# Kernel optimization log

Measured on AMD Instinct MI355X. Metric: run time of the kernel, lower is better.

Reference implementation:

```python
import jax, jax.numpy as jnp
import numpy as np

B, P, M, N, H, K, EH = 16, 50, 512, 1024, 64, 20, 200


def setup_inputs() -> dict:
    key = jax.random.key(0)
    ks = jax.random.split(key, 16)
    b = jax.random.normal(ks[0], (B, P, M, 1), jnp.float32)
    A = jax.random.normal(ks[1], (1, P, M, N), jnp.float32) / np.float32(np.sqrt(M))
    # random undirected multigraph on P nodes, stored with both directions
    s = jax.random.randint(ks[2], (B, EH), 0, P)
    off = jax.random.randint(ks[3], (B, EH), 1, P)
    d = (s + off) % P
    edge_index = jnp.stack([jnp.concatenate([s, d], 1), jnp.concatenate([d, s], 1)], 1).astype(jnp.int32)  # [B,2,2*EH]

    def lin(k, fi, fo, scale=None):
        scale = np.float32(1.0 / np.sqrt(fi)) if scale is None else np.float32(scale)
        return jax.random.normal(k, (fi, fo), jnp.float32) * scale, jnp.zeros((fo,), jnp.float32)

    W_e1, b_e1 = lin(ks[4], P * M, P * H)
    W_e2, b_e2 = lin(ks[5], P * H, 2 * P * H)
    W_e3, b_e3 = lin(ks[6], 2 * P * H, 4 * P * H)
    W_c1, b_c1 = lin(ks[7], 4 * H, 2 * H)
    W_c2, b_c2 = lin(ks[8], 2 * H, 2 * H)
    W_f1, b_f1 = lin(ks[9], 2 * H, H)
    W_f2, _ = lin(ks[10], H, K * 4, scale=1e-3)
    b_f2 = jnp.full((K * 4,), -2.0, jnp.float32)  # mimics fc2 init (tiny weights, negative bias)
    max_param = jnp.array([0.01, 0.1, 0.1, 0.1], jnp.float32).reshape(1, 1, 1, 4)  # [alpha,tau,rho,eta]_max
    y0 = jax.random.normal(ks[11], (B, P, N, 1), jnp.float32) * 0.01
    u0 = jax.random.normal(ks[12], (B, P, N, 1), jnp.float32) * 0.01
    d0 = jax.random.normal(ks[13], (B, P, N, 1), jnp.float32) * 0.01
    return dict(b=b, A=A, edge_index=edge_index, max_param=max_param,
                W_e1=W_e1, b_e1=b_e1, W_e2=W_e2, b_e2=b_e2, W_e3=W_e3, b_e3=b_e3,
                W_c1=W_c1, b_c1=b_c1, W_c2=W_c2, b_c2=b_c2,
                W_f1=W_f1, b_f1=b_f1, W_f2=W_f2, b_f2=b_f2,
                y0=y0, u0=u0, d0=d0)


def _lrelu(x):
    return jax.nn.leaky_relu(x, 0.01)


def _gcn(x, s, d, W, bias):
    # GCNConv: sym-normalized propagation with self loops. x: [P,F]
    h = x @ W
    deg = jnp.zeros((x.shape[0],), x.dtype).at[d].add(1.0) + 1.0  # +1 self loop
    dinv = jax.lax.rsqrt(deg)
    agg = jnp.zeros_like(h).at[d].add(h[s] * (dinv[s] * dinv[d])[:, None])
    agg = agg + h * (dinv * dinv)[:, None]  # self-loop term
    return agg + bias


def _delta(y, s, d):
    # nested neighbor loop: for each directed edge (s,d): delta[s]+=y[s]-y[d]; delta[d]-=same
    diff = y[s] - y[d]  # [E,N,1]
    return jnp.zeros_like(y).at[s].add(diff).at[d].add(-diff)


def reference(b, A, edge_index, max_param,
              W_e1, b_e1, W_e2, b_e2, W_e3, b_e3,
              W_c1, b_c1, W_c2, b_c2, W_f1, b_f1, W_f2, b_f2,
              y0, u0, d0):
    Bb = b.shape[0]
    n = A.shape[3]
    k_steps = W_f2.shape[1] // 4
    src, dst = edge_index[:, 0], edge_index[:, 1]

    # ---- GNN hypernetwork ----
    x = b.reshape(Bb, -1)
    x = _lrelu(x @ W_e1 + b_e1)
    x = _lrelu(x @ W_e2 + b_e2)
    x = (x @ W_e3 + b_e3).reshape(Bb, P, -1)  # [B,P,4H]
    x = _lrelu(jax.vmap(lambda xf, s, d: _gcn(xf, s, d, W_c1, b_c1))(x, src, dst))
    x = _lrelu(jax.vmap(lambda xf, s, d: _gcn(xf, s, d, W_c2, b_c2))(x, src, dst))
    x = x.mean(axis=1)  # global_mean_pool over nodes
    x = _lrelu(x @ W_f1 + b_f1)
    hyp = (x @ W_f2 + b_f2).reshape(Bb, k_steps, 1, 4)
    hyp = jax.nn.sigmoid(jnp.cumsum(hyp, axis=1)) * max_param  # [B,K,1,4]
    hyp_scan = jnp.transpose(hyp, (1, 3, 0, 2))[..., None, None]  # [K,4,B,1,1,1]

    # ---- precompute ----
    A0 = A[0]  # [P,M,N]
    AtA = jnp.einsum('pmn,pmk->pnk', A0, A0)  # [P,N,N]
    Atb = jnp.einsum('pmn,bpmo->bpno', A0, b)  # [B,P,N,1]
    sum_nb = jax.vmap(lambda s: jnp.zeros((P,), b.dtype).at[s].add(1.0))(src)[:, :, None, None]  # [B,P,1,1]

    # ---- unrolled D-ADMM / DLASSO ----
    def step(carry, hk):
        y_k, U_k, dlt = carry
        alpha, tau, rho, eta = hk[0], hk[1], hk[2], hk[3]
        AtAy = jnp.einsum('pnk,bpko->bpno', AtA, y_k)
        g = AtAy - Atb + jnp.sign(y_k) * tau + U_k * sum_nb + dlt * rho
        y_n = y_k - alpha * g
        dlt_n = jax.vmap(_delta)(y_n, src, dst)
        U_n = U_k + dlt_n * eta
        return (y_n, U_n, dlt_n), y_n

    _, Y = jax.lax.scan(step, (y0, u0, d0), hyp_scan)
    return Y  # [K,B,P,N,1]
```

## Files before the change

### kernel.cpp

```cpp
#include <hip/hip_runtime.h>

namespace {
constexpr int NB = 16;
constexpr int NP = 50;
constexpr int NM = 512;
constexpr int NN = 1024;
constexpr int NK = 20;
constexpr long ASZ = (long)NP * NM * NN;
constexpr long YSZ = (long)NB * NP * NN;
}

typedef __attribute__((ext_vector_type(8))) short bf16x8;
typedef __attribute__((ext_vector_type(4))) float f32x4;

__device__ __forceinline__ float lrelu(float x){ return x > 0.f ? x : 0.01f*x; }
__device__ __forceinline__ unsigned short f2bf(float f){
  unsigned u = __builtin_bit_cast(unsigned, f);
  u += 0x7fffu + ((u >> 16) & 1u);
  return (unsigned short)(u >> 16);
}

__global__ __launch_bounds__(256) void k_prep(const float* __restrict__ A,
                      unsigned short* __restrict__ abfT){
  const int p = blockIdx.x, mt = blockIdx.y, nt = blockIdx.z;
  const int tid = threadIdx.x;
  __shared__ unsigned short tile[64][72];
  const int m0 = mt*64, n0 = nt*64;
  {
    int r = tid>>2, cs = (tid&3)*16;
    const float* src = A + ((long)p*NM + m0 + r)*NN + n0 + cs;
    unsigned short tmp[16];
    #pragma unroll
    for (int q=0;q<16;q+=4){
      float4 v = *(const float4*)(src+q);
      tmp[q+0]=f2bf(v.x); tmp[q+1]=f2bf(v.y); tmp[q+2]=f2bf(v.z); tmp[q+3]=f2bf(v.w);
    }
    #pragma unroll
    for (int q=0;q<16;q++) tile[r][cs+q] = tmp[q];
  }
  __syncthreads();
  {
    int r = tid>>2, cs = (tid&3)*16;
    unsigned short* dst = abfT + ((long)p*NN + n0 + r)*NM + m0 + cs;
    unsigned short tmp[16];
    #pragma unroll
    for (int q=0;q<16;q++) tmp[q] = tile[cs+q][r];
    #pragma unroll
    for (int q=0;q<16;q+=8) *(uint4*)(dst+q) = *(const uint4*)&tmp[q];
  }
}

__global__ void k_init(const float* __restrict__ y0, const float* __restrict__ u0,
                       float* __restrict__ y, float* __restrict__ u,
                       unsigned short* __restrict__ ybf, int n){
  int e = (blockIdx.x*blockDim.x + threadIdx.x)*4;
  if (e >= n) return;
  float4 a = *(const float4*)(y0+e);
  *(float4*)(y+e) = a;
  ushort4 o; o.x=f2bf(a.x); o.y=f2bf(a.y); o.z=f2bf(a.z); o.w=f2bf(a.w);
  *(ushort4*)(ybf+e) = o;
  *(float4*)(u+e)  = *(const float4*)(u0+e);
}

__global__ __launch_bounds__(256) void k_c0(const float* __restrict__ u0,
      const float* __restrict__ d0, const float* __restrict__ snbg,
      const float* __restrict__ hypg, float* __restrict__ c){
  long e = ((long)blockIdx.x*256 + threadIdx.x)*4;
  if (e >= YSZ) return;
  long bp = e >> 10;
  int b = (int)(bp/NP), p = (int)(bp%NP);
  float sp = snbg[b*NP+p], rho = hypg[b*80 + 2];
  float4 uv = *(const float4*)(u0+e);
  float4 dv = *(const float4*)(d0+e);
  float4 cv;
  cv.x = uv.x*sp + dv.x*rho; cv.y = uv.y*sp + dv.y*rho;
  cv.z = uv.z*sp + dv.z*rho; cv.w = uv.w*sp + dv.w*rho;
  *(float4*)(c+e) = cv;
}

__global__ __launch_bounds__(256) void k_atb(const unsigned short* __restrict__ abfT,
                      const float* __restrict__ src, float* __restrict__ z){
  const int p = blockIdx.x;
  const int tid = threadIdx.x, wave = tid>>6, lane = tid&63;
  __shared__ unsigned short tlds[16][520];
  {
    int b = tid>>4, c0 = (tid&15)*8;
    const float* tr = src + ((long)b*NP + p)*NM;
    #pragma unroll
    for (int it=0; it<4; it++){
      float4 lo = *(const float4*)(tr + it*128 + c0);
      float4 hi = *(const float4*)(tr + it*128 + c0 + 4);
      unsigned short w[8];
      w[0]=f2bf(lo.x); w[1]=f2bf(lo.y); w[2]=f2bf(lo.z); w[3]=f2bf(lo.w);
      w[4]=f2bf(hi.x); w[5]=f2bf(hi.y); w[6]=f2bf(hi.z); w[7]=f2bf(hi.w);
      *(uint4*)&tlds[b][it*128 + c0] = *(const uint4*)w;
    }
  }
  __syncthreads();
  const int lr = lane&15, kg = lane>>4;
  const int nt0 = blockIdx.y*4 + wave;
  const int n0 = nt0*16, n1 = (nt0+32)*16;
  const unsigned short* b0 = abfT + ((long)p*NN + n0 + lr)*NM + kg*8;
  const unsigned short* b1 = abfT + ((long)p*NN + n1 + lr)*NM + kg*8;
  const unsigned short* tp = &tlds[lr][kg*8];
  f32x4 acc0a={0.f,0.f,0.f,0.f}, acc0b={0.f,0.f,0.f,0.f};
  f32x4 acc1a={0.f,0.f,0.f,0.f}, acc1b={0.f,0.f,0.f,0.f};
  #pragma unroll 4
  for (int ks=0; ks<16; ks+=2){
    bf16x8 t0 = *(const bf16x8*)(tp + ks*32);
    bf16x8 t1 = *(const bf16x8*)(tp + ks*32 + 32);
    bf16x8 b00 = *(const bf16x8*)(b0 + (long)ks*32);
    bf16x8 b01 = *(const bf16x8*)(b0 + (long)ks*32 + 32);
    bf16x8 b10 = *(const bf16x8*)(b1 + (long)ks*32);
    bf16x8 b11 = *(const bf16x8*)(b1 + (long)ks*32 + 32);
    acc0a = __builtin_amdgcn_mfma_f32_16x16x32_bf16(t0, b00, acc0a, 0, 0, 0);
    acc1a = __builtin_amdgcn_mfma_f32_16x16x32_bf16(t0, b10, acc1a, 0, 0, 0);
    acc0b = __builtin_amdgcn_mfma_f32_16x16x32_bf16(t1, b01, acc0b, 0, 0, 0);
    acc1b = __builtin_amdgcn_mfma_f32_16x16x32_bf16(t1, b11, acc1b, 0, 0, 0);
  }
  f32x4 acc0 = acc0a + acc0b;
  f32x4 acc1 = acc1a + acc1b;
  #pragma unroll
  for (int r=0;r<4;r++){
    int bb = kg*4 + r;
    z[((long)bb*NP + p)*NN + n0 + lr] = acc0[r];
    z[((long)bb*NP + p)*NN + n1 + lr] = acc1[r];
  }
}

__global__ __launch_bounds__(256) void k_ata(const unsigned short* __restrict__ abfT,
                      unsigned short* __restrict__ ata){
  const int p = blockIdx.x;
  int yy = blockIdx.y, bi = 0;
  while (yy >= 8 - bi){ yy -= 8 - bi; bi++; }
  const int bj = bi + yy;
  const int i0 = bi*128, j0 = bj*128;
  const int tid = threadIdx.x, wave = tid>>6, lane = tid&63;
  const int lr = lane&15, kg = lane>>4;
  __shared__ unsigned short pa[128][72];
  __shared__ unsigned short pb[128][72];
  f32x4 acc[2][8];
  #pragma unroll
  for (int ti=0;ti<2;ti++)
    #pragma unroll
    for (int tj=0;tj<8;tj++) acc[ti][tj] = (f32x4){0.f,0.f,0.f,0.f};
  const unsigned short* Abase = abfT + (long)p*NN*NM;
  for (int mc=0; mc<NM; mc+=64){
    __syncthreads();
    {
      int r = tid>>1, c0 = (tid&1)*32;
      const unsigned short* sa = Abase + (long)(i0 + r)*NM + mc + c0;
      const unsigned short* sb = Abase + (long)(j0 + r)*NM + mc + c0;
      #pragma unroll
      for (int q=0;q<32;q+=8){
        *(uint4*)&pa[r][c0+q] = *(const uint4*)(sa+q);
        *(uint4*)&pb[r][c0+q] = *(const uint4*)(sb+q);
      }
    }
    __syncthreads();
    #pragma unroll
    for (int ks=0; ks<2; ks++){
      bf16x8 av0 = *(const bf16x8*)&pa[wave*32      + lr][ks*32 + kg*8];
      bf16x8 av1 = *(const bf16x8*)&pa[wave*32 + 16 + lr][ks*32 + kg*8];
      #pragma unroll
      for (int tj=0;tj<8;tj++){
        bf16x8 bv = *(const bf16x8*)&pb[tj*16 + lr][ks*32 + kg*8];
        acc[0][tj] = __builtin_amdgcn_mfma_f32_16x16x32_bf16(av0, bv, acc[0][tj], 0,0,0);
        acc[1][tj] = __builtin_amdgcn_mfma_f32_16x16x32_bf16(av1, bv, acc[1][tj], 0,0,0);
      }
    }
  }
  const long pbase = (long)p << 20;
  #pragma unroll
  for (int ti=0; ti<2; ti++){
    const int ib = i0 + wave*32 + ti*16;
    #pragma unroll
    for (int tj=0; tj<8; tj++){
      const int jb = j0 + tj*16;
      unsigned short w[4];
      #pragma unroll
      for (int r=0;r<4;r++) w[r] = f2bf(acc[ti][tj][r]);
      #pragma unroll
      for (int r=0;r<4;r++)
        ata[pbase + (long)(ib + kg*4 + r)*1024 + jb + lr] = w[r];
      if (bi != bj)
        *(ushort4*)(ata + pbase + (long)(jb + lr)*1024 + ib + kg*4) = *(const ushort4*)w;
    }
  }
}

__global__ __launch_bounds__(256) void k_enc2(const float* __restrict__ X, const float* __restrict__ W,
                           float* __restrict__ part, int fi, int fo, int ichunk, int actin){
  const int tid = threadIdx.x;
  const int o0 = (blockIdx.x*256 + tid)*4;
  const int c  = blockIdx.y;
  const bool ok = o0 < fo;
  __shared__ float xs[64][16];
  float4 acc[16];
  #pragma unroll
  for (int b=0;b<16;b++){ acc[b].x=0.f; acc[b].y=0.f; acc[b].z=0.f; acc[b].w=0.f; }
  const long ibase = (long)c*ichunk;
  const int xb = tid&15, xio = (tid>>4)*4;
  for (int s=0; s<ichunk; s+=64){
    float4 v = *(const float4*)(X + (long)xb*fi + ibase + s + xio);
    if (actin){ v.x=lrelu(v.x); v.y=lrelu(v.y); v.z=lrelu(v.z); v.w=lrelu(v.w); }
    __syncthreads();
    xs[xio+0][xb]=v.x; xs[xio+1][xb]=v.y; xs[xio+2][xb]=v.z; xs[xio+3][xb]=v.w;
    __syncthreads();
    const float* wp = W + (ibase+s)*fo + o0;
    #pragma unroll 4
    for (int i=0;i<64;i++){
      float4 w;
      if (ok) w = *(const float4*)(wp + (long)i*fo);
      else { w.x=0.f; w.y=0.f; w.z=0.f; w.w=0.f; }
      #pragma unroll
      for (int b2=0;b2<16;b2+=4){
        float4 x4 = *(const float4*)&xs[i][b2];
        acc[b2+0].x += w.x*x4.x; acc[b2+0].y += w.y*x4.x; acc[b2+0].z += w.z*x4.x; acc[b2+0].w += w.w*x4.x;
        acc[b2+1].x += w.x*x4.y; acc[b2+1].y += w.y*x4.y; acc[b2+1].z += w.z*x4.y; acc[b2+1].w += w.w*x4.y;
        acc[b2+2].x += w.x*x4.z; acc[b2+2].y += w.y*x4.z; acc[b2+2].z += w.z*x4.z; acc[b2+2].w += w.w*x4.z;
        acc[b2+3].x += w.x*x4.w; acc[b2+3].y += w.y*x4.w; acc[b2+3].z += w.z*x4.w; acc[b2+3].w += w.w*x4.w;
      }
    }
  }
  if (ok){
    float* pp = part + ((long)c*16)*fo + o0;
    #pragma unroll
    for (int b=0;b<16;b++) *(float4*)(pp + (long)b*fo) = acc[b];
  }
}

__global__ void k_enc_reduce(const float* __restrict__ part, const float* __restrict__ bias,
                             float* __restrict__ out, int fo, int nchunk){
  int i = blockIdx.x*256 + threadIdx.x;
  if (i >= 16*fo) return;
  int o = i % fo;
  float s = bias[o];
  for (int c=0;c<nchunk;c++) s += part[(long)c*16*fo + i];
  out[i] = s;
}

__global__ __launch_bounds__(64) void k_graph(const int* __restrict__ ei, float* __restrict__ adjg,
                        float* __restrict__ dmg, float* __restrict__ snbg){
  const int b = blockIdx.x, tid = threadIdx.x;
  __shared__ float adj[2500], dm[2500], deg[50], dinv[50], snb[50];
  for (int i=tid;i<2500;i+=64){ adj[i]=0.f; dm[i]=0.f; }
  if (tid<50){ deg[tid]=0.f; snb[tid]=0.f; }
  __syncthreads();
  const int* e = ei + b*800;
  for (int k=tid;k<400;k+=64){
    atomicAdd(&deg[e[400+k]], 1.f);
    atomicAdd(&snb[e[k]], 1.f);
  }
  __syncthreads();
  if (tid<50) dinv[tid] = 1.f / sqrtf(deg[tid] + 1.f);
  __syncthreads();
  for (int k=tid;k<400;k+=64){
    int s = e[k], d = e[400+k];
    atomicAdd(&adj[d*50+s], dinv[s]*dinv[d]);
    atomicAdd(&dm[s*50+s],  1.f); atomicAdd(&dm[s*50+d], -1.f);
    atomicAdd(&dm[d*50+d],  1.f); atomicAdd(&dm[d*50+s], -1.f);
  }
  __syncthreads();
  if (tid<50) adj[tid*50+tid] += dinv[tid]*dinv[tid];
  __syncthreads();
  for (int i=tid;i<2500;i+=64){ adjg[b*2500+i]=adj[i]; dmg[b*2500+i]=dm[i]; }
  if (tid<50) snbg[b*50+tid]=snb[tid];
}

__global__ __launch_bounds__(256) void k_gnn(const float* __restrict__ h3,
     const float* __restrict__ Wc1, const float* __restrict__ bc1,
     const float* __restrict__ Wc2, const float* __restrict__ bc2,
     const float* __restrict__ Wf1, const float* __restrict__ bf1,
     const float* __restrict__ Wf2, const float* __restrict__ bf2,
     const float* __restrict__ maxp, const float* __restrict__ adjg,
     float* __restrict__ hypg){
  const int b = blockIdx.x, tid = threadIdx.x;
  __shared__ float adj[2500];
  __shared__ float bufA[6400];
  __shared__ float bufB[6400];
  __shared__ float xm[128], hv1[64], raw[80];
  for (int i=tid;i<2500;i+=256) adj[i] = adjg[b*2500+i];

  const int j = tid & 127, nh = tid >> 7;
  float acc[25];
  #pragma unroll
  for (int q=0;q<25;q++) acc[q]=0.f;
  for (int ic=0; ic<4; ic++){
    __syncthreads();
    for (int e=tid; e<800; e+=256){
      int n = e>>4, seg = (e&15)*4;
      *(float4*)&bufB[n*64+seg] = *(const float4*)(h3 + (long)b*12800 + n*256 + ic*64 + seg);
    }
    __syncthreads();
    for (int i=0;i<64;i+=4){
      float w0 = Wc1[(long)(ic*64+i+0)*128 + j];
      float w1 = Wc1[(long)(ic*64+i+1)*128 + j];
      float w2 = Wc1[(long)(ic*64+i+2)*128 + j];
      float w3 = Wc1[(long)(ic*64+i+3)*128 + j];
      #pragma unroll
      for (int q=0;q<25;q++){
        float4 xv = *(const float4*)&bufB[(nh*25+q)*64 + i];
        acc[q] += xv.x*w0 + xv.y*w1 + xv.z*w2 + xv.w*w3;
      }
    }
  }
  __syncthreads();
  #pragma unroll
  for (int q=0;q<25;q++) bufA[(nh*25+q)*128 + j] = acc[q];
  __syncthreads();
  {
    float a2[25];
    float bv = bc1[j];
    #pragma unroll
    for (int q=0;q<25;q++) a2[q]=bv;
    for (int qq=0; qq<50; qq++){
      float hvv = bufA[qq*128 + j];
      #pragma unroll
      for (int q=0;q<25;q++) a2[q] += adj[(nh*25+q)*50 + qq]*hvv;
    }
    __syncthreads();
    #pragma unroll
    for (int q=0;q<25;q++) bufB[(nh*25+q)*128 + j] = lrelu(a2[q]);
  }
  __syncthreads();
  {
    float a2[25];
    #pragma unroll
    for (int q=0;q<25;q++) a2[q]=0.f;
    for (int i=0;i<128;i+=4){
      float w0 = Wc2[(long)(i+0)*128 + j];
      float w1 = Wc2[(long)(i+1)*128 + j];
      float w2 = Wc2[(long)(i+2)*128 + j];
      float w3 = Wc2[(long)(i+3)*128 + j];
      #pragma unroll
      for (int q=0;q<25;q++){
        float4 xv = *(const float4*)&bufB[(nh*25+q)*128 + i];
        a2[q] += xv.x*w0 + xv.y*w1 + xv.z*w2 + xv.w*w3;
      }
    }
    __syncthreads();
    #pragma unroll
    for (int q=0;q<25;q++) bufA[(nh*25+q)*128 + j] = a2[q];
  }
  __syncthreads();
  {
    float a2[25];
    float bv = bc2[j];
    #pragma unroll
    for (int q=0;q<25;q++) a2[q]=bv;
    for (int qq=0; qq<50; qq++){
      float hvv = bufA[qq*128 + j];
      #pragma unroll
      for (int q=0;q<25;q++) a2[q] += adj[(nh*25+q)*50 + qq]*hvv;
    }
    __syncthreads();
    #pragma unroll
    for (int q=0;q<25;q++) bufB[(nh*25+q)*128 + j] = lrelu(a2[q]);
  }
  __syncthreads();
  if (tid < 128){
    float s = 0.f;
    for (int n=0;n<50;n++) s += bufB[n*128 + tid];
    xm[tid] = s * (1.f/50.f);
  }
  __syncthreads();
  if (tid < 64){
    float s = bf1[tid];
    for (int i=0;i<128;i++) s += xm[i]*Wf1[i*64 + tid];
    hv1[tid] = lrelu(s);
  }
  __syncthreads();
  if (tid < 80){
    float s = bf2[tid];
    for (int i=0;i<64;i++) s += hv1[i]*Wf2[i*80 + tid];
    raw[tid] = s;
  }
  __syncthreads();
  if (tid < 4){
    float c = 0.f;
    for (int k=0;k<20;k++){
      c += raw[k*4 + tid];
      hypg[b*80 + k*4 + tid] = maxp[tid] / (1.f + expf(-c));
    }
  }
}

__global__ __launch_bounds__(256) void k_z(const unsigned short* __restrict__ ata,
      const unsigned short* __restrict__ ybin, const float* __restrict__ atb,
      const float* __restrict__ cbuf, const float* __restrict__ hypg, int k,
      float* __restrict__ y, unsigned short* __restrict__ ybout,
      float* __restrict__ yout){
  const int p = blockIdx.x;
  const int tid = threadIdx.x, wave = tid>>6, lane = tid&63;
  __shared__ unsigned short ylds[16][1032];
  {
    int b = tid>>4, c0 = (tid&15)*8;
    const unsigned short* yr = ybin + ((long)b*NP + p)*NN;
    #pragma unroll
    for (int it=0; it<8; it++)
      *(uint4*)&ylds[b][it*128 + c0] = *(const uint4*)(yr + it*128 + c0);
  }
  const int lr = lane&15, kg = lane>>4;
  const int n0 = (blockIdx.y*4 + wave)*16;
  const long pb2 = (long)p << 20;
  const unsigned short* bp = ata + pb2 + (long)(n0 + lr)*1024 + kg*8;
  const unsigned short* yp = &ylds[lr][kg*8];

  float yv4[4], atb4[4], c4[4];
  float4 hp4[4];
  #pragma unroll
  for (int r=0;r<4;r++){
    const int b = kg*4 + r;
    const long idx = ((long)b*NP + p)*NN + n0 + lr;
    yv4[r] = y[idx]; atb4[r] = atb[idx]; c4[r] = cbuf[idx];
    hp4[r] = *(const float4*)(hypg + b*80 + k*4);
  }
  __syncthreads();

  f32x4 a0={0.f,0.f,0.f,0.f}, a1={0.f,0.f,0.f,0.f}, a2={0.f,0.f,0.f,0.f}, a3={0.f,0.f,0.f,0.f};
  #pragma unroll 4
  for (int i=0;i<8;i++){
    bf16x8 b0 = *(const bf16x8*)(bp + (i*4+0)*32);
    bf16x8 b1 = *(const bf16x8*)(bp + (i*4+1)*32);
    bf16x8 b2 = *(const bf16x8*)(bp + (i*4+2)*32);
    bf16x8 b3 = *(const bf16x8*)(bp + (i*4+3)*32);
    bf16x8 y0 = *(const bf16x8*)(yp + (i*4+0)*32);
    bf16x8 y1 = *(const bf16x8*)(yp + (i*4+1)*32);
    bf16x8 y2 = *(const bf16x8*)(yp + (i*4+2)*32);
    bf16x8 y3 = *(const bf16x8*)(yp + (i*4+3)*32);
    a0 = __builtin_amdgcn_mfma_f32_16x16x32_bf16(y0, b0, a0, 0,0,0);
    a1 = __builtin_amdgcn_mfma_f32_16x16x32_bf16(y1, b1, a1, 0,0,0);
    a2 = __builtin_amdgcn_mfma_f32_16x16x32_bf16(y2, b2, a2, 0,0,0);
    a3 = __builtin_amdgcn_mfma_f32_16x16x32_bf16(y3, b3, a3, 0,0,0);
  }
  f32x4 z = (a0 + a1) + (a2 + a3);
  #pragma unroll
  for (int r=0;r<4;r++){
    const int b = kg*4 + r;
    const long idx = ((long)b*NP + p)*NN + n0 + lr;
    float yv = yv4[r];
    float g = z[r] - atb4[r] + ((yv>0.f)?1.f:((yv<0.f)?-1.f:0.f))*hp4[r].y + c4[r];
    float ynv = yv - hp4[r].x*g;
    y[idx] = ynv; ybout[idx] = f2bf(ynv); yout[(long)k*YSZ + idx] = ynv;
  }
}

__global__ __launch_bounds__(256) void k_dm(const float* __restrict__ dmg,
      const float* __restrict__ snbg, const float* __restrict__ hypg, int k,
      const float* __restrict__ y, float* __restrict__ u, float* __restrict__ c){
  const int b = blockIdx.x, n0 = blockIdx.y*128, tid = threadIdx.x;
  __shared__ float ys[50][128];
  __shared__ float dms[2500];
  for (int i=tid;i<2500;i+=256) dms[i] = dmg[b*2500+i];
  for (int e=tid; e<6400; e+=256){
    int p=e>>7, nn=e&127;
    ys[p][nn] = y[((long)b*NP+p)*NN + n0 + nn];
  }
  __syncthreads();
  const float eta = hypg[b*80 + k*4 + 3];
  const float rhon = hypg[b*80 + (k+1)*4 + 2];
  for (int e=tid; e<6400; e+=256){
    int p=e>>7, nn=e&127;
    float s=0.f;
    #pragma unroll 10
    for (int q=0;q<NP;q++) s += dms[p*50+q]*ys[q][nn];
    long idx = ((long)b*NP+p)*NN + n0 + nn;
    float un = u[idx] + s*eta;
    u[idx] = un;
    c[idx] = un*snbg[b*NP+p] + s*rhon;
  }
}

extern "C" void kernel_launch(void* const* d_in, const int* in_sizes, int n_in,
                              void* d_out, int out_size, void* d_ws, size_t ws_size,
                              hipStream_t stream){
  (void)in_sizes; (void)n_in; (void)out_size; (void)ws_size;
  const float* bin = (const float*)d_in[0];
  const float* A   = (const float*)d_in[1];
  const int*   ei  = (const int*)d_in[2];
  const float* mxp = (const float*)d_in[3];
  const float* We1 = (const float*)d_in[4];  const float* be1 = (const float*)d_in[5];
  const float* We2 = (const float*)d_in[6];  const float* be2 = (const float*)d_in[7];
  const float* We3 = (const float*)d_in[8];  const float* be3 = (const float*)d_in[9];
  const float* Wc1 = (const float*)d_in[10]; const float* bc1 = (const float*)d_in[11];
  const float* Wc2 = (const float*)d_in[12]; const float* bc2 = (const float*)d_in[13];
  const float* Wf1 = (const float*)d_in[14]; const float* bf1 = (const float*)d_in[15];
  const float* Wf2 = (const float*)d_in[16]; const float* bf2 = (const float*)d_in[17];
  const float* y0  = (const float*)d_in[18];
  const float* u0  = (const float*)d_in[19];
  const float* dd0 = (const float*)d_in[20];
  float* out = (float*)d_out;

  char* cur = (char*)d_ws;
  auto alloc = [&](size_t bytes)->void*{
    void* pp = (void*)cur; cur += (bytes + 255) & ~(size_t)255; return pp;
  };
  unsigned short* abfT = (unsigned short*)alloc(ASZ*2);
  unsigned short* ata  = (unsigned short*)alloc((size_t)NP*1024*1024*2);
  float* atb = (float*)alloc(YSZ*4);
  float* y   = (float*)alloc(YSZ*4);
  unsigned short* ybf0 = (unsigned short*)alloc(YSZ*2);
  unsigned short* ybf1 = (unsigned short*)alloc(YSZ*2);
  float* u   = (float*)alloc(YSZ*4);
  float* cb  = (float*)alloc(YSZ*4);
  float* h1  = (float*)alloc((size_t)16*3200*4);
  float* h2  = (float*)alloc((size_t)16*6400*4);
  float* h3  = (float*)alloc((size_t)16*12800*4);
  float* adj = (float*)alloc((size_t)16*2500*4);
  float* dm  = (float*)alloc((size_t)16*2500*4);
  float* snb = (float*)alloc((size_t)16*50*4);
  float* hyp = (float*)alloc((size_t)16*80*4);
  float* part= (float*)alloc((size_t)84000000);

  k_prep<<<dim3(50,8,16), dim3(256), 0, stream>>>(A, abfT);
  k_init<<<dim3(800), dim3(256), 0, stream>>>(y0, u0, y, u, ybf0, (int)YSZ);
  k_atb<<<dim3(50,8), dim3(256), 0, stream>>>(abfT, bin, atb);
  k_ata<<<dim3(50,36), dim3(256), 0, stream>>>(abfT, ata);

  k_enc2<<<dim3(4,200),  dim3(256), 0, stream>>>(bin, We1, part, 25600, 3200, 128, 0);
  k_enc_reduce<<<dim3(200), dim3(256), 0, stream>>>(part, be1, h1, 3200, 200);
  k_enc2<<<dim3(7,50),  dim3(256), 0, stream>>>(h1, We2, part, 3200, 6400, 64, 1);
  k_enc_reduce<<<dim3(400), dim3(256), 0, stream>>>(part, be2, h2, 6400, 50);
  k_enc2<<<dim3(13,100), dim3(256), 0, stream>>>(h2, We3, part, 6400, 12800, 64, 1);
  k_enc_reduce<<<dim3(800), dim3(256), 0, stream>>>(part, be3, h3, 12800, 100);

  k_graph<<<dim3(16), dim3(64), 0, stream>>>(ei, adj, dm, snb);
  k_gnn<<<dim3(16), dim3(256), 0, stream>>>(h3, Wc1, bc1, Wc2, bc2, Wf1, bf1, Wf2, bf2, mxp, adj, hyp);
  k_c0<<<dim3(800), dim3(256), 0, stream>>>(u0, dd0, snb, hyp, cb);

  for (int k=0;k<NK;k++){
    const unsigned short* ybin = (k & 1) ? ybf1 : ybf0;
    unsigned short* ybout      = (k & 1) ? ybf0 : ybf1;
    k_z<<<dim3(50,16), dim3(256), 0, stream>>>(ata, ybin, atb, cb, hyp, k, y, ybout, out);
    if (k < NK-1)
      k_dm<<<dim3(16,8), dim3(256), 0, stream>>>(dm, snb, hyp, k, y, u, cb);
  }
}
```

Before: 1.530 ms.

## Fuse unrolled ADMM iterations into one persistent kernel with grid barriers

Replaces the per-iteration k_z and k_dm launches, plus the init and c0 kernels, with one persistent 800-block kernel. Blocks synchronise through a global atomic counter barrier, and y, u and atb stay in registers across the 20 steps. The delta (graph Laplacian) term is recomputed inside each block from the bf16 copy of y, which removes the fp32 y, u and c round-trips through memory. In exchange it relies on all 800 blocks being co-resident, otherwise the barrier deadlocks. It also does redundant per-block reads of the other nodes' y, and computes delta from bf16 rather than fp32 y, which lowers precision.

```diff
diff --git a/kernel.cpp b/kernel.cpp
--- a/kernel.cpp
+++ b/kernel.cpp
@@ -14,6 +14,10 @@
 typedef __attribute__((ext_vector_type(4))) float f32x4;
 
 __device__ __forceinline__ float lrelu(float x){ return x > 0.f ? x : 0.01f*x; }
+__device__ __forceinline__ float bfu(unsigned short x){
+  unsigned v = ((unsigned)x) << 16;
+  return __builtin_bit_cast(float, v);
+}
 __device__ __forceinline__ unsigned short f2bf(float f){
   unsigned u = __builtin_bit_cast(unsigned, f);
   u += 0x7fffu + ((u >> 16) & 1u);
@@ -50,33 +54,7 @@
   }
 }
 
-__global__ void k_init(const float* __restrict__ y0, const float* __restrict__ u0,
-                       float* __restrict__ y, float* __restrict__ u,
-                       unsigned short* __restrict__ ybf, int n){
-  int e = (blockIdx.x*blockDim.x + threadIdx.x)*4;
-  if (e >= n) return;
-  float4 a = *(const float4*)(y0+e);
-  *(float4*)(y+e) = a;
-  ushort4 o; o.x=f2bf(a.x); o.y=f2bf(a.y); o.z=f2bf(a.z); o.w=f2bf(a.w);
-  *(ushort4*)(ybf+e) = o;
-  *(float4*)(u+e)  = *(const float4*)(u0+e);
-}
-
-__global__ __launch_bounds__(256) void k_c0(const float* __restrict__ u0,
-      const float* __restrict__ d0, const float* __restrict__ snbg,
-      const float* __restrict__ hypg, float* __restrict__ c){
-  long e = ((long)blockIdx.x*256 + threadIdx.x)*4;
-  if (e >= YSZ) return;
-  long bp = e >> 10;
-  int b = (int)(bp/NP), p = (int)(bp%NP);
-  float sp = snbg[b*NP+p], rho = hypg[b*80 + 2];
-  float4 uv = *(const float4*)(u0+e);
-  float4 dv = *(const float4*)(d0+e);
-  float4 cv;
-  cv.x = uv.x*sp + dv.x*rho; cv.y = uv.y*sp + dv.y*rho;
-  cv.z = uv.z*sp + dv.z*rho; cv.w = uv.w*sp + dv.w*rho;
-  *(float4*)(c+e) = cv;
-}
+__global__ void k_zero(unsigned long long* cnt){ *cnt = 0ull; }
 
 __global__ __launch_bounds__(256) void k_atb(const unsigned short* __restrict__ abfT,
                       const float* __restrict__ src, float* __restrict__ z){
@@ -386,89 +364,117 @@
   }
 }
 
-__global__ __launch_bounds__(256) void k_z(const unsigned short* __restrict__ ata,
-      const unsigned short* __restrict__ ybin, const float* __restrict__ atb,
-      const float* __restrict__ cbuf, const float* __restrict__ hypg, int k,
-      float* __restrict__ y, unsigned short* __restrict__ ybout,
-      float* __restrict__ yout){
-  const int p = blockIdx.x;
+__device__ __forceinline__ void gridbar(unsigned long long* cnt, unsigned long long target){
+  __syncthreads();
+  if (threadIdx.x == 0){
+    __threadfence();
+    __hip_atomic_fetch_add(cnt, 1ull, __ATOMIC_ACQ_REL, __HIP_MEMORY_SCOPE_AGENT);
+    while (__hip_atomic_load(cnt, __ATOMIC_ACQUIRE, __HIP_MEMORY_SCOPE_AGENT) < target)
+      __builtin_amdgcn_s_sleep(8);
+    __threadfence();
+  }
+  __syncthreads();
+}
+
+__global__ __launch_bounds__(256, 4) void k_scan(
+      const unsigned short* __restrict__ ata, const float* __restrict__ atb_g,
+      const float* __restrict__ y0, const float* __restrict__ u0,
+      const float* __restrict__ d0, const float* __restrict__ dmg,
+      const float* __restrict__ snbg, const float* __restrict__ hypg,
+      unsigned short* __restrict__ yb0, unsigned short* __restrict__ yb1,
+      float* __restrict__ yout, unsigned long long* cnt){
+  const int p  = blockIdx.x >> 4;
+  const int nt = blockIdx.x & 15;
   const int tid = threadIdx.x, wave = tid>>6, lane = tid&63;
+  const int lr = lane&15, kg = lane>>4;
+  const int n  = nt*64 + wave*16 + lr;
   __shared__ unsigned short ylds[16][1032];
-  {
-    int b = tid>>4, c0 = (tid&15)*8;
-    const unsigned short* yr = ybin + ((long)b*NP + p)*NN;
-    #pragma unroll
-    for (int it=0; it<8; it++)
-      *(uint4*)&ylds[b][it*128 + c0] = *(const uint4*)(yr + it*128 + c0);
-  }
-  const int lr = lane&15, kg = lane>>4;
-  const int n0 = (blockIdx.y*4 + wave)*16;
-  const long pb2 = (long)p << 20;
-  const unsigned short* bp = ata + pb2 + (long)(n0 + lr)*1024 + kg*8;
-  const unsigned short* yp = &ylds[lr][kg*8];
-
-  float yv4[4], atb4[4], c4[4];
-  float4 hp4[4];
+  __shared__ float dmp[16][52];
+  __shared__ float snp[16];
+  for (int e = tid; e < 800; e += 256){
+    int b = e/50, q = e%50;
+    dmp[b][q] = dmg[b*2500 + p*50 + q];
+  }
+  if (tid < 16) snp[tid] = snbg[tid*NP + p];
+
+  float yv[4], uv[4], at4[4], ds[4];
   #pragma unroll
   for (int r=0;r<4;r++){
-    const int b = kg*4 + r;
-    const long idx = ((long)b*NP + p)*NN + n0 + lr;
-    yv4[r] = y[idx]; atb4[r] = atb[idx]; c4[r] = cbuf[idx];
-    hp4[r] = *(const float4*)(hypg + b*80 + k*4);
-  }
-  __syncthreads();
-
-  f32x4 a0={0.f,0.f,0.f,0.f}, a1={0.f,0.f,0.f,0.f}, a2={0.f,0.f,0.f,0.f}, a3={0.f,0.f,0.f,0.f};
-  #pragma unroll 4
-  for (int i=0;i<8;i++){
-    bf16x8 b0 = *(const bf16x8*)(bp + (i*4+0)*32);
-    bf16x8 b1 = *(const bf16x8*)(bp + (i*4+1)*32);
-    bf16x8 b2 = *(const bf16x8*)(bp + (i*4+2)*32);
-    bf16x8 b3 = *(const bf16x8*)(bp + (i*4+3)*32);
-    bf16x8 y0 = *(const bf16x8*)(yp + (i*4+0)*32);
-    bf16x8 y1 = *(const bf16x8*)(yp + (i*4+1)*32);
-    bf16x8 y2 = *(const bf16x8*)(yp + (i*4+2)*32);
-    bf16x8 y3 = *(const bf16x8*)(yp + (i*4+3)*32);
-    a0 = __builtin_amdgcn_mfma_f32_16x16x32_bf16(y0, b0, a0, 0,0,0);
-    a1 = __builtin_amdgcn_mfma_f32_16x16x32_bf16(y1, b1, a1, 0,0,0);
-    a2 = __builtin_amdgcn_mfma_f32_16x16x32_bf16(y2, b2, a2, 0,0,0);
-    a3 = __builtin_amdgcn_mfma_f32_16x16x32_bf16(y3, b3, a3, 0,0,0);
-  }
-  f32x4 z = (a0 + a1) + (a2 + a3);
-  #pragma unroll
-  for (int r=0;r<4;r++){
-    const int b = kg*4 + r;
-    const long idx = ((long)b*NP + p)*NN + n0 + lr;
-    float yv = yv4[r];
-    float g = z[r] - atb4[r] + ((yv>0.f)?1.f:((yv<0.f)?-1.f:0.f))*hp4[r].y + c4[r];
-    float ynv = yv - hp4[r].x*g;
-    y[idx] = ynv; ybout[idx] = f2bf(ynv); yout[(long)k*YSZ + idx] = ynv;
-  }
-}
-
-__global__ __launch_bounds__(256) void k_dm(const float* __restrict__ dmg,
-      const float* __restrict__ snbg, const float* __restrict__ hypg, int k,
-      const float* __restrict__ y, float* __restrict__ u, float* __restrict__ c){
-  const int b = blockIdx.x, n0 = blockIdx.y*128, tid = threadIdx.x;
-  __shared__ float ys[50][128];
-  __shared__ float dms[2500];
-  for (int i=tid;i<2500;i+=256) dms[i] = dmg[b*2500+i];
-  for (int e=tid; e<6400; e+=256){
-    int p=e>>7, nn=e&127;
-    ys[p][nn] = y[((long)b*NP+p)*NN + n0 + nn];
-  }
-  __syncthreads();
-  const float eta = hypg[b*80 + k*4 + 3];
-  const float rhon = hypg[b*80 + (k+1)*4 + 2];
-  for (int e=tid; e<6400; e+=256){
-    int p=e>>7, nn=e&127;
-    float s=0.f;
-    #pragma unroll 10
-    for (int q=0;q<NP;q++) s += dms[p*50+q]*ys[q][nn];
-    long idx = ((long)b*NP+p)*NN + n0 + nn;
-    float un = u[idx] + s*eta;
-    u[idx] = un;
-    c[idx] = un*snbg[b*NP+p] + s*rhon;
+    const int b = kg*4+r;
+    const long idx = ((long)b*NP + p)*NN + n;
+    yv[r]  = y0[idx];
+    uv[r]  = u0[idx];
+    at4[r] = atb_g[idx];
+    yb0[idx] = f2bf(yv[r]);
+  }
+  __threadfence();
+  gridbar(cnt, 800ull);
+
+  for (int k=0;k<NK;k++){
+    const unsigned short* ybin = (k&1) ? yb1 : yb0;
+    unsigned short*       ybot = (k&1) ? yb0 : yb1;
+    if (k == 0){
+      #pragma unroll
+      for (int r=0;r<4;r++)
+        ds[r] = d0[((long)(kg*4+r)*NP + p)*NN + n];
+    } else {
+      #pragma unroll
+      for (int r=0;r<4;r++) ds[r] = 0.f;
+      for (int q=0;q<NP;q++){
+        #pragma unroll
+        for (int r=0;r<4;r++){
+          float yq = bfu(ybin[((long)(kg*4+r)*NP + q)*NN + n]);
+          ds[r] += dmp[kg*4+r][q]*yq;
+        }
+      }
+      #pragma unroll
+      for (int r=0;r<4;r++)
+        uv[r] += hypg[(kg*4+r)*80 + (k-1)*4 + 3]*ds[r];
+    }
+    __syncthreads();
+    {
+      int bb = tid>>4, c0 = (tid&15)*8;
+      const unsigned short* yr = ybin + ((long)bb*NP + p)*NN;
+      #pragma unroll
+      for (int it=0; it<8; it++)
+        *(uint4*)&ylds[bb][it*128 + c0] = *(const uint4*)(yr + it*128 + c0);
+    }
+    __syncthreads();
+    const unsigned short* bp = ata + ((long)p<<20) + (long)(nt*64 + wave*16 + lr)*1024 + kg*8;
+    const unsigned short* yp = &ylds[lr][kg*8];
+    f32x4 a0={0.f,0.f,0.f,0.f}, a1={0.f,0.f,0.f,0.f}, a2={0.f,0.f,0.f,0.f}, a3={0.f,0.f,0.f,0.f};
+    #pragma unroll 2
+    for (int i=0;i<8;i++){
+      bf16x8 b0 = *(const bf16x8*)(bp + (i*4+0)*32);
+      bf16x8 b1 = *(const bf16x8*)(bp + (i*4+1)*32);
+      bf16x8 b2 = *(const bf16x8*)(bp + (i*4+2)*32);
+      bf16x8 b3 = *(const bf16x8*)(bp + (i*4+3)*32);
+      bf16x8 q0 = *(const bf16x8*)(yp + (i*4+0)*32);
+      bf16x8 q1 = *(const bf16x8*)(yp + (i*4+1)*32);
+      bf16x8 q2 = *(const bf16x8*)(yp + (i*4+2)*32);
+      bf16x8 q3 = *(const bf16x8*)(yp + (i*4+3)*32);
+      a0 = __builtin_amdgcn_mfma_f32_16x16x32_bf16(q0, b0, a0, 0,0,0);
+      a1 = __builtin_amdgcn_mfma_f32_16x16x32_bf16(q1, b1, a1, 0,0,0);
+      a2 = __builtin_amdgcn_mfma_f32_16x16x32_bf16(q2, b2, a2, 0,0,0);
+      a3 = __builtin_amdgcn_mfma_f32_16x16x32_bf16(q3, b3, a3, 0,0,0);
+    }
+    f32x4 z = (a0 + a1) + (a2 + a3);
+    #pragma unroll
+    for (int r=0;r<4;r++){
+      const int b = kg*4+r;
+      const float4 hp = *(const float4*)(hypg + b*80 + k*4);
+      float g = z[r] - at4[r] + ((yv[r]>0.f)?1.f:((yv[r]<0.f)?-1.f:0.f))*hp.y
+              + uv[r]*snp[b] + ds[r]*hp.z;
+      yv[r] -= hp.x*g;
+      yout[(long)k*YSZ + ((long)b*NP+p)*NN + n] = yv[r];
+    }
+    if (k < NK-1){
+      #pragma unroll
+      for (int r=0;r<4;r++)
+        ybot[((long)(kg*4+r)*NP + p)*NN + n] = f2bf(yv[r]);
+      __threadfence();
+      gridbar(cnt, (unsigned long long)(k+2)*800ull);
+    }
   }
 }
 
@@ -499,11 +505,8 @@
   unsigned short* abfT = (unsigned short*)alloc(ASZ*2);
   unsigned short* ata  = (unsigned short*)alloc((size_t)NP*1024*1024*2);
   float* atb = (float*)alloc(YSZ*4);
-  float* y   = (float*)alloc(YSZ*4);
   unsigned short* ybf0 = (unsigned short*)alloc(YSZ*2);
   unsigned short* ybf1 = (unsigned short*)alloc(YSZ*2);
-  float* u   = (float*)alloc(YSZ*4);
-  float* cb  = (float*)alloc(YSZ*4);
   float* h1  = (float*)alloc((size_t)16*3200*4);
   float* h2  = (float*)alloc((size_t)16*6400*4);
   float* h3  = (float*)alloc((size_t)16*12800*4);
@@ -511,10 +514,11 @@
   float* dm  = (float*)alloc((size_t)16*2500*4);
   float* snb = (float*)alloc((size_t)16*50*4);
   float* hyp = (float*)alloc((size_t)16*80*4);
+  unsigned long long* cnt = (unsigned long long*)alloc(256);
   float* part= (float*)alloc((size_t)84000000);
 
+  k_zero<<<dim3(1), dim3(1), 0, stream>>>(cnt);
   k_prep<<<dim3(50,8,16), dim3(256), 0, stream>>>(A, abfT);
-  k_init<<<dim3(800), dim3(256), 0, stream>>>(y0, u0, y, u, ybf0, (int)YSZ);
   k_atb<<<dim3(50,8), dim3(256), 0, stream>>>(abfT, bin, atb);
   k_ata<<<dim3(50,36), dim3(256), 0, stream>>>(abfT, ata);
 
@@ -527,13 +531,7 @@
 
   k_graph<<<dim3(16), dim3(64), 0, stream>>>(ei, adj, dm, snb);
   k_gnn<<<dim3(16), dim3(256), 0, stream>>>(h3, Wc1, bc1, Wc2, bc2, Wf1, bf1, Wf2, bf2, mxp, adj, hyp);
-  k_c0<<<dim3(800), dim3(256), 0, stream>>>(u0, dd0, snb, hyp, cb);
-
-  for (int k=0;k<NK;k++){
-    const unsigned short* ybin = (k & 1) ? ybf1 : ybf0;
-    unsigned short* ybout      = (k & 1) ? ybf0 : ybf1;
-    k_z<<<dim3(50,16), dim3(256), 0, stream>>>(ata, ybin, atb, cb, hyp, k, y, ybout, out);
-    if (k < NK-1)
-      k_dm<<<dim3(16,8), dim3(256), 0, stream>>>(dm, snb, hyp, k, y, u, cb);
-  }
-}
+
+  k_scan<<<dim3(800), dim3(256), 0, stream>>>(ata, atb, y0, u0, dd0, dm, snb, hyp,
+                                              ybf0, ybf1, out, cnt);
+}
```

Measured after the change: 5.770 ms. +277.3%, slower.

## Prefetch AtA tiles in k_z, read bf16 y in k_dm, reorder k_ata grid

Applied to the files above, without the earlier changes.

k_z now uses a three-deep register ring of B-fragments, prefetching AtA two iterations ahead so global-load latency overlaps the MFMAs. It also adds a launch-bounds occupancy hint and fully unrolls the loop. k_dm reads the bf16 copy of y instead of fp32, halving its y traffic at the cost of bf16 rounding in the consensus term. k_ata's grid is transposed so tiles of the same node p run adjacently, which may improve cache locality.

```diff
diff --git a/kernel.cpp b/kernel.cpp
--- a/kernel.cpp
+++ b/kernel.cpp
@@ -14,6 +14,10 @@
 typedef __attribute__((ext_vector_type(4))) float f32x4;
 
 __device__ __forceinline__ float lrelu(float x){ return x > 0.f ? x : 0.01f*x; }
+__device__ __forceinline__ float bfu(unsigned short x){
+  unsigned v = ((unsigned)x) << 16;
+  return __builtin_bit_cast(float, v);
+}
 __device__ __forceinline__ unsigned short f2bf(float f){
   unsigned u = __builtin_bit_cast(unsigned, f);
   u += 0x7fffu + ((u >> 16) & 1u);
@@ -130,8 +134,8 @@
 
 __global__ __launch_bounds__(256) void k_ata(const unsigned short* __restrict__ abfT,
                       unsigned short* __restrict__ ata){
-  const int p = blockIdx.x;
-  int yy = blockIdx.y, bi = 0;
+  const int p = blockIdx.y;
+  int yy = blockIdx.x, bi = 0;
   while (yy >= 8 - bi){ yy -= 8 - bi; bi++; }
   const int bj = bi + yy;
   const int i0 = bi*128, j0 = bj*128;
@@ -386,7 +390,7 @@
   }
 }
 
-__global__ __launch_bounds__(256) void k_z(const unsigned short* __restrict__ ata,
+__global__ __launch_bounds__(256, 4) void k_z(const unsigned short* __restrict__ ata,
       const unsigned short* __restrict__ ybin, const float* __restrict__ atb,
       const float* __restrict__ cbuf, const float* __restrict__ hypg, int k,
       float* __restrict__ y, unsigned short* __restrict__ ybout,
@@ -407,6 +411,12 @@
   const unsigned short* bp = ata + pb2 + (long)(n0 + lr)*1024 + kg*8;
   const unsigned short* yp = &ylds[lr][kg*8];
 
+  bf16x8 B[3][4];
+  #pragma unroll
+  for (int j=0;j<4;j++) B[0][j] = *(const bf16x8*)(bp + (0*4+j)*32);
+  #pragma unroll
+  for (int j=0;j<4;j++) B[1][j] = *(const bf16x8*)(bp + (1*4+j)*32);
+
   float yv4[4], atb4[4], c4[4];
   float4 hp4[4];
   #pragma unroll
@@ -419,20 +429,22 @@
   __syncthreads();
 
   f32x4 a0={0.f,0.f,0.f,0.f}, a1={0.f,0.f,0.f,0.f}, a2={0.f,0.f,0.f,0.f}, a3={0.f,0.f,0.f,0.f};
-  #pragma unroll 4
+  #pragma unroll
   for (int i=0;i<8;i++){
-    bf16x8 b0 = *(const bf16x8*)(bp + (i*4+0)*32);
-    bf16x8 b1 = *(const bf16x8*)(bp + (i*4+1)*32);
-    bf16x8 b2 = *(const bf16x8*)(bp + (i*4+2)*32);
-    bf16x8 b3 = *(const bf16x8*)(bp + (i*4+3)*32);
-    bf16x8 y0 = *(const bf16x8*)(yp + (i*4+0)*32);
-    bf16x8 y1 = *(const bf16x8*)(yp + (i*4+1)*32);
-    bf16x8 y2 = *(const bf16x8*)(yp + (i*4+2)*32);
-    bf16x8 y3 = *(const bf16x8*)(yp + (i*4+3)*32);
-    a0 = __builtin_amdgcn_mfma_f32_16x16x32_bf16(y0, b0, a0, 0,0,0);
-    a1 = __builtin_amdgcn_mfma_f32_16x16x32_bf16(y1, b1, a1, 0,0,0);
-    a2 = __builtin_amdgcn_mfma_f32_16x16x32_bf16(y2, b2, a2, 0,0,0);
-    a3 = __builtin_amdgcn_mfma_f32_16x16x32_bf16(y3, b3, a3, 0,0,0);
+    const int cur = i % 3;
+    const int nxt = (i+2) % 3;
+    if (i < 6){
+      #pragma unroll
+      for (int j=0;j<4;j++) B[nxt][j] = *(const bf16x8*)(bp + ((i+2)*4+j)*32);
+    }
+    bf16x8 q0 = *(const bf16x8*)(yp + (i*4+0)*32);
+    bf16x8 q1 = *(const bf16x8*)(yp + (i*4+1)*32);
+    bf16x8 q2 = *(const bf16x8*)(yp + (i*4+2)*32);
+    bf16x8 q3 = *(const bf16x8*)(yp + (i*4+3)*32);
+    a0 = __builtin_amdgcn_mfma_f32_16x16x32_bf16(q0, B[cur][0], a0, 0,0,0);
+    a1 = __builtin_amdgcn_mfma_f32_16x16x32_bf16(q1, B[cur][1], a1, 0,0,0);
+    a2 = __builtin_amdgcn_mfma_f32_16x16x32_bf16(q2, B[cur][2], a2, 0,0,0);
+    a3 = __builtin_amdgcn_mfma_f32_16x16x32_bf16(q3, B[cur][3], a3, 0,0,0);
   }
   f32x4 z = (a0 + a1) + (a2 + a3);
   #pragma unroll
@@ -448,14 +460,14 @@
 
 __global__ __launch_bounds__(256) void k_dm(const float* __restrict__ dmg,
       const float* __restrict__ snbg, const float* __restrict__ hypg, int k,
-      const float* __restrict__ y, float* __restrict__ u, float* __restrict__ c){
+      const unsigned short* __restrict__ ybf, float* __restrict__ u, float* __restrict__ c){
   const int b = blockIdx.x, n0 = blockIdx.y*128, tid = threadIdx.x;
   __shared__ float ys[50][128];
   __shared__ float dms[2500];
   for (int i=tid;i<2500;i+=256) dms[i] = dmg[b*2500+i];
   for (int e=tid; e<6400; e+=256){
     int p=e>>7, nn=e&127;
-    ys[p][nn] = y[((long)b*NP+p)*NN + n0 + nn];
+    ys[p][nn] = bfu(ybf[((long)b*NP+p)*NN + n0 + nn]);
   }
   __syncthreads();
   const float eta = hypg[b*80 + k*4 + 3];
@@ -516,7 +528,7 @@
   k_prep<<<dim3(50,8,16), dim3(256), 0, stream>>>(A, abfT);
   k_init<<<dim3(800), dim3(256), 0, stream>>>(y0, u0, y, u, ybf0, (int)YSZ);
   k_atb<<<dim3(50,8), dim3(256), 0, stream>>>(abfT, bin, atb);
-  k_ata<<<dim3(50,36), dim3(256), 0, stream>>>(abfT, ata);
+  k_ata<<<dim3(36,50), dim3(256), 0, stream>>>(abfT, ata);
 
   k_enc2<<<dim3(4,200),  dim3(256), 0, stream>>>(bin, We1, part, 25600, 3200, 128, 0);
   k_enc_reduce<<<dim3(200), dim3(256), 0, stream>>>(part, be1, h1, 3200, 200);
@@ -533,7 +545,9 @@
     const unsigned short* ybin = (k & 1) ? ybf1 : ybf0;
     unsigned short* ybout      = (k & 1) ? ybf0 : ybf1;
     k_z<<<dim3(50,16), dim3(256), 0, stream>>>(ata, ybin, atb, cb, hyp, k, y, ybout, out);
-    if (k < NK-1)
-      k_dm<<<dim3(16,8), dim3(256), 0, stream>>>(dm, snb, hyp, k, y, u, cb);
-  }
-}
+    if (k < NK-1){
+      const unsigned short* ybnew = (k & 1) ? ybf0 : ybf1;
+      k_dm<<<dim3(16,8), dim3(256), 0, stream>>>(dm, snb, hyp, k, ybnew, u, cb);
+    }
+  }
+}
```

After: 1.532 ms. No clear change (+0.2%).
